# Kernel optimization log

Hardware: AMD Instinct MI355X
Metric: run time of the kernel (lower is better)

Reference implementation:

```python
import jax, jax.numpy as jnp
import numpy as np
from jax import lax

DIM = 128          # embedding dim
LG = 3             # layer_gnn
LC = 3             # layer_cnn
LO = 2             # layer_output
WIN = 11           # window -> conv kernel 23x23, padding 11 (SAME)
NF = 10000         # n_fingerprint
NW = 10000         # n_word
NA = 4096          # n_atoms
NWORDS = 16384     # protein length


def setup_inputs() -> dict:
    key = jax.random.key(0)
    ks = jax.random.split(key, 16)
    s = 1.0 / np.sqrt(DIM)
    s2 = 1.0 / np.sqrt(2 * DIM)
    K = 2 * WIN + 1
    return {
        "fingerprints": jax.random.randint(ks[0], (NA,), 0, NF),
        # sparse-ish binary adjacency like a molecular graph, scaled up
        "adjacency": (jax.random.uniform(ks[1], (NA, NA)) < 0.005).astype(jnp.float32),
        "words": jax.random.randint(ks[2], (NWORDS,), 0, NW),
        "emb_fp": jax.random.normal(ks[3], (NF, DIM), dtype=jnp.float32) * 0.1,
        "emb_word": jax.random.normal(ks[4], (NW, DIM), dtype=jnp.float32) * 0.1,
        "W_gnn_w": jax.random.normal(ks[5], (LG, DIM, DIM), dtype=jnp.float32) * s,
        "W_gnn_b": jax.random.normal(ks[6], (LG, DIM), dtype=jnp.float32) * s,
        "conv_w": jax.random.normal(ks[7], (LC, 1, 1, K, K), dtype=jnp.float32) * 0.02,
        "conv_b": jax.random.normal(ks[8], (LC, 1), dtype=jnp.float32) * 0.02,
        "W_att_w": jax.random.normal(ks[9], (DIM, DIM), dtype=jnp.float32) * s,
        "W_att_b": jax.random.normal(ks[10], (DIM,), dtype=jnp.float32) * s,
        "W_out_w": jax.random.normal(ks[11], (LO, 2 * DIM, 2 * DIM), dtype=jnp.float32) * s2,
        "W_out_b": jax.random.normal(ks[12], (LO, 2 * DIM), dtype=jnp.float32) * s2,
        "W_int_w": jax.random.normal(ks[13], (1, 2 * DIM), dtype=jnp.float32) * s2,
        "W_int_b": jax.random.normal(ks[14], (1,), dtype=jnp.float32) * s2,
    }


def _linear(x, w, b):
    # torch nn.Linear: y = x @ w.T + b
    return x @ w.T + b


def reference(fingerprints, adjacency, words, emb_fp, emb_word,
              W_gnn_w, W_gnn_b, conv_w, conv_b, W_att_w, W_att_b,
              W_out_w, W_out_b, W_int_w, W_int_b):
    # ---- Compound vector with GNN ----
    xs = emb_fp[fingerprints]                      # [NA, DIM]
    for l in range(LG):
        hs = jax.nn.relu(_linear(xs, W_gnn_w[l], W_gnn_b[l]))
        xs = xs + adjacency @ hs                   # residual message passing
    compound = jnp.mean(xs, axis=0, keepdims=True) # [1, DIM]

    # ---- Protein vector with attention-CNN ----
    ws = emb_word[words]                           # [NWORDS, DIM]
    img = ws[None, None]                           # [1, 1, NWORDS, DIM]
    for l in range(LC):
        img = lax.conv_general_dilated(
            img, conv_w[l], window_strides=(1, 1), padding='SAME',
            dimension_numbers=('NCHW', 'OIHW', 'NCHW'))
        img = img + conv_b[l].reshape(1, -1, 1, 1)
        img = jax.nn.leaky_relu(img, negative_slope=0.01)
    ws = img[0, 0]                                 # [NWORDS, DIM]

    h = jax.nn.relu(_linear(compound, W_att_w, W_att_b))   # [1, DIM]
    hs = jax.nn.relu(_linear(ws, W_att_w, W_att_b))        # [NWORDS, DIM]
    weights = jnp.tanh(h @ hs.T)                            # [1, NWORDS]
    ys = weights.T * hs                                     # [NWORDS, DIM]
    protein = jnp.mean(ys, axis=0, keepdims=True)           # [1, DIM]

    # ---- Concatenate and output ----
    cat = jnp.concatenate((compound, protein), axis=1)      # [1, 2*DIM]
    for l in range(LO):
        cat = jax.nn.relu(_linear(cat, W_out_w[l], W_out_b[l]))
    interaction = _linear(cat, W_int_w, W_int_b)            # [1, 1]
    return interaction
```

## Files before the change

### kernel.cpp

```cpp
#include <hip/hip_runtime.h>

#define DIM 128
#define NA 4096
#define NWORDS 16384
#define MAXNZ 256
#define KW 23
#define PAD 11

__global__ void k_gather(float* __restrict__ out, const float* __restrict__ tab,
                         const int* __restrict__ idx) {
  int t = blockIdx.x * blockDim.x + threadIdx.x;
  int r = t >> 5, c = t & 31;
  ((float4*)out)[t] = ((const float4*)(tab + (size_t)idx[r] * DIM))[c];
}

__global__ void k_adj_scan(int* __restrict__ cnt, int* __restrict__ colx,
                           float* __restrict__ valx, const float* __restrict__ adj) {
  int w = threadIdx.x >> 6, lane = threadIdx.x & 63;
  int row = blockIdx.x * 4 + w;
  const float4* ar = (const float4*)(adj + (size_t)row * NA);
  int count = 0;
  unsigned long long ltm = (1ull << lane) - 1ull;
  for (int c4 = lane; c4 < NA / 4; c4 += 64) {
    float4 v = ar[c4];
    #pragma unroll
    for (int e = 0; e < 4; ++e) {
      float ve = e == 0 ? v.x : e == 1 ? v.y : e == 2 ? v.z : v.w;
      unsigned long long m = __ballot(ve != 0.0f);
      if (ve != 0.0f) {
        int off = count + (int)__popcll(m & ltm);
        if (off < MAXNZ) { colx[row * MAXNZ + off] = c4 * 4 + e; valx[row * MAXNZ + off] = ve; }
      }
      count += (int)__popcll(m);
    }
  }
  if (lane == 0) cnt[row] = count;
}

__global__ __launch_bounds__(256) void k_linear_relu(
    float* __restrict__ out, const float* __restrict__ A,
    const float* __restrict__ W, const float* __restrict__ bias) {
  __shared__ float As[64 * 132];
  __shared__ float Ws[64 * 132];
  int mt = blockIdx.x >> 1, nt = blockIdx.x & 1;
  int r0 = mt * 64, c0 = nt * 64;
  int tid = threadIdx.x;
  for (int q = tid; q < 64 * 32; q += 256) {
    int row = q >> 5, c4 = q & 31;
    *(float4*)&As[row * 132 + c4 * 4] = *(const float4*)&A[(size_t)(r0 + row) * DIM + c4 * 4];
    *(float4*)&Ws[row * 132 + c4 * 4] = *(const float4*)&W[(size_t)(c0 + row) * DIM + c4 * 4];
  }
  __syncthreads();
  int rgr = tid & 15, cgr = tid >> 4;
  float acc[4][4] = {};
  #pragma unroll 4
  for (int k4 = 0; k4 < 32; ++k4) {
    int kk = ((k4 + rgr) & 31) * 4;
    float4 a[4], w[4];
    #pragma unroll
    for (int i = 0; i < 4; ++i) a[i] = *(const float4*)&As[(rgr * 4 + i) * 132 + kk];
    #pragma unroll
    for (int j = 0; j < 4; ++j) w[j] = *(const float4*)&Ws[(cgr * 4 + j) * 132 + kk];
    #pragma unroll
    for (int i = 0; i < 4; ++i)
      #pragma unroll
      for (int j = 0; j < 4; ++j)
        acc[i][j] += a[i].x * w[j].x + a[i].y * w[j].y + a[i].z * w[j].z + a[i].w * w[j].w;
  }
  #pragma unroll
  for (int i = 0; i < 4; ++i) {
    int r = r0 + rgr * 4 + i;
    int c = c0 + cgr * 4;
    float4 bv = *(const float4*)&bias[c];
    float4 o;
    o.x = acc[i][0] + bv.x; o.y = acc[i][1] + bv.y;
    o.z = acc[i][2] + bv.z; o.w = acc[i][3] + bv.w;
    o.x = o.x > 0.f ? o.x : 0.f; o.y = o.y > 0.f ? o.y : 0.f;
    o.z = o.z > 0.f ? o.z : 0.f; o.w = o.w > 0.f ? o.w : 0.f;
    *(float4*)&out[(size_t)r * DIM + c] = o;
  }
}

__global__ void k_spmm(float* __restrict__ xs, const float* __restrict__ hs,
                       const int* __restrict__ cnt, const int* __restrict__ colx,
                       const float* __restrict__ valx, const float* __restrict__ adj) {
  __shared__ int scol[MAXNZ];
  __shared__ float sval[MAXNZ];
  int r = blockIdx.x, d = threadIdx.x;
  int n = cnt[r];
  int m = (n <= MAXNZ) ? n : 0;
  for (int i = d; i < m; i += 128) {
    scol[i] = colx[r * MAXNZ + i];
    sval[i] = valx[r * MAXNZ + i];
  }
  __syncthreads();
  float acc = xs[(size_t)r * DIM + d];
  if (n <= MAXNZ) {
    for (int i = 0; i < n; ++i)
      acc += sval[i] * hs[(size_t)scol[i] * DIM + d];
  } else {
    for (int c = 0; c < NA; ++c) {
      float a = adj[(size_t)r * NA + c];
      if (a != 0.f) acc += a * hs[(size_t)c * DIM + d];
    }
  }
  xs[(size_t)r * DIM + d] = acc;
}

__global__ void k_mean(float* __restrict__ out, const float* __restrict__ in,
                       int rows_per_block, float scale) {
  __shared__ float red[256];
  int d = threadIdx.x & 127, half = threadIdx.x >> 7;
  int r0 = blockIdx.x * rows_per_block;
  float acc = 0.f;
  for (int r = r0 + half; r < r0 + rows_per_block; r += 2)
    acc += in[(size_t)r * DIM + d];
  red[threadIdx.x] = acc;
  __syncthreads();
  if (half == 0) atomicAdd(&out[d], (acc + red[threadIdx.x + 128]) * scale);
}

#define CROWS 16
#define TROWS 38
#define TCOLS 150
#define TSTR  150
__global__ __launch_bounds__(256) void k_conv(
    float* __restrict__ out, const float* __restrict__ in,
    const float* __restrict__ cw, const float* __restrict__ cb) {
  __shared__ float tile[TROWS * TSTR];
  int r0 = blockIdx.x * CROWS;
  int tid = threadIdx.x;
  for (int p = tid; p < TROWS * TCOLS; p += 256) {
    int rr = p / TCOLS, cc = p - rr * TCOLS;
    int gr = r0 - PAD + rr, gc = cc - PAD;
    float v = 0.f;
    if ((unsigned)gr < NWORDS && (unsigned)gc < DIM) v = in[(size_t)gr * DIM + gc];
    tile[rr * TSTR + cc] = v;
  }
  __syncthreads();
  int col = tid & 127, rb = tid >> 7;
  int rbase = rb * 8;
  float acc[8] = {};
  for (int dx = 0; dx < KW; ++dx) {
    float v[30];
    #pragma unroll
    for (int j = 0; j < 30; ++j)
      v[j] = tile[(rbase + j) * TSTR + col + dx];
    const float* wp = cw + dx;
    #pragma unroll
    for (int dy = 0; dy < KW; ++dy) {
      float wv = wp[dy * KW];
      #pragma unroll
      for (int i = 0; i < 8; ++i) acc[i] += wv * v[i + dy];
    }
  }
  float bias = cb[0];
  #pragma unroll
  for (int i = 0; i < 8; ++i) {
    float x = acc[i] + bias;
    out[(size_t)(r0 + rbase + i) * DIM + col] = x > 0.f ? x : 0.01f * x;
  }
}

__global__ __launch_bounds__(256) void k_attprot(
    float* __restrict__ prot, const float* __restrict__ hsA,
    const float* __restrict__ comp, const float* __restrict__ W,
    const float* __restrict__ b) {
  __shared__ float cvec[DIM];
  __shared__ float hv_s[DIM];
  __shared__ float lw[32];
  __shared__ float red[256];
  int tid = threadIdx.x;
  int w = tid >> 6, lane = tid & 63;
  if (tid < 128) cvec[tid] = comp[tid];
  __syncthreads();
  if (tid < 128) {
    float acc = b[tid];
    #pragma unroll
    for (int k4 = 0; k4 < 32; ++k4) {
      float4 w4 = *(const float4*)&W[tid * DIM + k4 * 4];
      acc += cvec[k4*4+0] * w4.x + cvec[k4*4+1] * w4.y + cvec[k4*4+2] * w4.z + cvec[k4*4+3] * w4.w;
    }
    hv_s[tid] = acc > 0.f ? acc : 0.f;
  }
  __syncthreads();
  int r0 = blockIdx.x * 32;
  float2 hv = ((const float2*)hv_s)[lane];
  for (int rr = w; rr < 32; rr += 4) {
    float2 xv = ((const float2*)(hsA + (size_t)(r0 + rr) * DIM))[lane];
    float dt = hv.x * xv.x + hv.y * xv.y;
    for (int o = 32; o > 0; o >>= 1) dt += __shfl_xor(dt, o);
    if (lane == 0) lw[rr] = tanhf(dt);
  }
  __syncthreads();
  int d = tid & 127, half = tid >> 7;
  float acc = 0.f;
  for (int rr = half; rr < 32; rr += 2)
    acc += lw[rr] * hsA[(size_t)(r0 + rr) * DIM + d];
  red[tid] = acc;
  __syncthreads();
  if (half == 0) atomicAdd(&prot[d], (acc + red[tid + 128]) * (1.f / NWORDS));
}

__global__ __launch_bounds__(256) void k_final(
    float* __restrict__ out, const float* __restrict__ comp, const float* __restrict__ prot,
    const float* __restrict__ Wo, const float* __restrict__ bo,
    const float* __restrict__ Wi, const float* __restrict__ bi) {
  __shared__ float cat[256];
  __shared__ float wred[4];
  int t = threadIdx.x;
  int w = t >> 6, lane = t & 63;
  cat[t] = t < 128 ? comp[t] : prot[t - 128];
  __syncthreads();
  for (int l = 0; l < 2; ++l) {
    const float* Wl = Wo + l * 256 * 256;
    float acc = bo[l * 256 + t];
    #pragma unroll 8
    for (int k4 = 0; k4 < 64; ++k4) {
      float4 w4 = *(const float4*)&Wl[t * 256 + k4 * 4];
      acc += cat[k4*4+0] * w4.x + cat[k4*4+1] * w4.y + cat[k4*4+2] * w4.z + cat[k4*4+3] * w4.w;
    }
    __syncthreads();
    cat[t] = acc > 0.f ? acc : 0.f;
    __syncthreads();
  }
  float r = cat[t] * Wi[t];
  for (int o = 32; o > 0; o >>= 1) r += __shfl_xor(r, o);
  if (lane == 0) wred[w] = r;
  __syncthreads();
  if (t == 0) out[0] = wred[0] + wred[1] + wred[2] + wred[3] + bi[0];
}

extern "C" void kernel_launch(void* const* d_in, const int* in_sizes, int n_in,
                              void* d_out, int out_size, void* d_ws, size_t ws_size,
                              hipStream_t stream) {
  const int*   fingerprints = (const int*)d_in[0];
  const float* adjacency    = (const float*)d_in[1];
  const int*   words        = (const int*)d_in[2];
  const float* emb_fp       = (const float*)d_in[3];
  const float* emb_word     = (const float*)d_in[4];
  const float* W_gnn_w      = (const float*)d_in[5];
  const float* W_gnn_b      = (const float*)d_in[6];
  const float* conv_w       = (const float*)d_in[7];
  const float* conv_b       = (const float*)d_in[8];
  const float* W_att_w      = (const float*)d_in[9];
  const float* W_att_b      = (const float*)d_in[10];
  const float* W_out_w      = (const float*)d_in[11];
  const float* W_out_b      = (const float*)d_in[12];
  const float* W_int_w      = (const float*)d_in[13];
  const float* W_int_b      = (const float*)d_in[14];
  float* out = (float*)d_out;

  float* xs   = (float*)d_ws;
  float* hsb  = xs   + 524288;
  float* valx = hsb  + 524288;
  float* pa   = valx + 1048576;
  float* pb   = pa   + 2097152;
  float* hsA  = pb   + 2097152;
  float* attw = hsA  + 2097152;
  float* small= attw + 16384;
  int*   colx = (int*)(small + 512);
  int*   cntv = colx + 1048576;
  float* comp = small, *prot = small + 128;
  (void)attw;

  hipMemsetAsync(small, 0, 512 * sizeof(float), stream);

  k_gather<<<512, 256, 0, stream>>>(xs, emb_fp, fingerprints);
  k_adj_scan<<<1024, 256, 0, stream>>>(cntv, colx, valx, adjacency);
  for (int l = 0; l < 3; ++l) {
    k_linear_relu<<<128, 256, 0, stream>>>(hsb, xs, W_gnn_w + l * DIM * DIM, W_gnn_b + l * DIM);
    k_spmm<<<NA, 128, 0, stream>>>(xs, hsb, cntv, colx, valx, adjacency);
  }
  k_mean<<<128, 256, 0, stream>>>(comp, xs, 32, 1.0f / NA);

  k_gather<<<2048, 256, 0, stream>>>(pa, emb_word, words);
  k_conv<<<1024, 256, 0, stream>>>(pb, pa, conv_w + 0 * 529, conv_b + 0);
  k_conv<<<1024, 256, 0, stream>>>(pa, pb, conv_w + 1 * 529, conv_b + 1);
  k_conv<<<1024, 256, 0, stream>>>(pb, pa, conv_w + 2 * 529, conv_b + 2);

  k_linear_relu<<<512, 256, 0, stream>>>(hsA, pb, W_att_w, W_att_b);
  k_attprot<<<512, 256, 0, stream>>>(prot, hsA, comp, W_att_w, W_att_b);

  k_final<<<1, 256, 0, stream>>>(out, comp, prot, W_out_w, W_out_b, W_int_w, W_int_b);
}
```

Before: 374.1 us.

## Restructure 23x23 conv to 2x4 register tiles with float4 LDS row loads

New measurement: 694.8 us. 1.86x slower.

```diff
diff --git a/kernel.cpp b/kernel.cpp
--- a/kernel.cpp
+++ b/kernel.cpp
@@ -122,9 +122,12 @@
 
 #define CROWS 16
 #define TROWS 38
-#define TCOLS 150
-#define TSTR  150
-__global__ __launch_bounds__(256) void k_conv(
+#define TCOLS 152
+#define TSTR  152
+__device__ __forceinline__ float f4get(const float4& v, int e) {
+  return e == 0 ? v.x : e == 1 ? v.y : e == 2 ? v.z : v.w;
+}
+__global__ __launch_bounds__(256, 4) void k_conv(
     float* __restrict__ out, const float* __restrict__ in,
     const float* __restrict__ cw, const float* __restrict__ cb) {
   __shared__ float tile[TROWS * TSTR];
@@ -132,34 +135,61 @@
   int tid = threadIdx.x;
   for (int p = tid; p < TROWS * TCOLS; p += 256) {
     int rr = p / TCOLS, cc = p - rr * TCOLS;
-    int gr = r0 - PAD + rr, gc = cc - PAD;
+    int gr = r0 - PAD + rr, gc = cc - 12;
     float v = 0.f;
     if ((unsigned)gr < NWORDS && (unsigned)gc < DIM) v = in[(size_t)gr * DIM + gc];
     tile[rr * TSTR + cc] = v;
   }
   __syncthreads();
-  int col = tid & 127, rb = tid >> 7;
-  int rbase = rb * 8;
-  float acc[8] = {};
-  for (int dx = 0; dx < KW; ++dx) {
-    float v[30];
-    #pragma unroll
-    for (int j = 0; j < 30; ++j)
-      v[j] = tile[(rbase + j) * TSTR + col + dx];
-    const float* wp = cw + dx;
-    #pragma unroll
-    for (int dy = 0; dy < KW; ++dy) {
-      float wv = wp[dy * KW];
-      #pragma unroll
-      for (int i = 0; i < 8; ++i) acc[i] += wv * v[i + dy];
-    }
-  }
+  int cg = tid & 31, rg = tid >> 5;
+  int c0 = cg * 4;
+  int orow = rg * 2;
+  float4 A[7], B[7];
+  float acc0[4] = {0.f, 0.f, 0.f, 0.f};
+  float acc1[4] = {0.f, 0.f, 0.f, 0.f};
+
+#define LOADROW(DST, trow) { \
+    const float4* p_ = (const float4*)&tile[(trow) * TSTR + c0]; \
+    _Pragma("unroll") for (int q = 0; q < 7; ++q) DST[q] = p_[q]; }
+
+#define CONV_STEP(R0, R1, wbase) { \
+    _Pragma("unroll") for (int dx = 0; dx < 23; ++dx) { \
+      float wv = (wbase)[dx]; \
+      _Pragma("unroll") for (int j = 0; j < 4; ++j) { \
+        int idx = 1 + j + dx; \
+        acc0[j] = __builtin_fmaf(wv, f4get(R0[idx >> 2], idx & 3), acc0[j]); \
+        acc1[j] = __builtin_fmaf(wv, f4get(R1[idx >> 2], idx & 3), acc1[j]); \
+      } } }
+
+  LOADROW(A, orow + 0)
+  LOADROW(B, orow + 1)
+  const float* wr = cw;
+  #pragma unroll 1
+  for (int d2 = 0; d2 < 11; ++d2) {
+    int dy = d2 * 2;
+    CONV_STEP(A, B, wr)
+    LOADROW(A, orow + dy + 2)
+    CONV_STEP(B, A, wr + KW)
+    LOADROW(B, orow + dy + 3)
+    wr += 2 * KW;
+  }
+  CONV_STEP(A, B, wr)
+#undef LOADROW
+#undef CONV_STEP
+
   float bias = cb[0];
-  #pragma unroll
-  for (int i = 0; i < 8; ++i) {
-    float x = acc[i] + bias;
-    out[(size_t)(r0 + rbase + i) * DIM + col] = x > 0.f ? x : 0.01f * x;
-  }
+  float4 o0, o1;
+  float x;
+  x = acc0[0] + bias; o0.x = x > 0.f ? x : 0.01f * x;
+  x = acc0[1] + bias; o0.y = x > 0.f ? x : 0.01f * x;
+  x = acc0[2] + bias; o0.z = x > 0.f ? x : 0.01f * x;
+  x = acc0[3] + bias; o0.w = x > 0.f ? x : 0.01f * x;
+  x = acc1[0] + bias; o1.x = x > 0.f ? x : 0.01f * x;
+  x = acc1[1] + bias; o1.y = x > 0.f ? x : 0.01f * x;
+  x = acc1[2] + bias; o1.z = x > 0.f ? x : 0.01f * x;
+  x = acc1[3] + bias; o1.w = x > 0.f ? x : 0.01f * x;
+  *(float4*)&out[(size_t)(r0 + orow + 0) * DIM + c0] = o0;
+  *(float4*)&out[(size_t)(r0 + orow + 1) * DIM + c0] = o1;
 }
 
 __global__ __launch_bounds__(256) void k_attprot(
```
